# Performance work log

Measured on AMD Instinct MI355X. Metric: run time of the kernel, lower is better.

The kernel has to match this reference:

```python
import jax, jax.numpy as jnp
import numpy as np
from jax import lax

# hyperparams (match init_kwargs)
DIM = 192      # dim
QK = 192       # qk_dim
HEADS = 8
GS = 128       # group_size
MLP = 384      # mlp_dim
M = 64         # num_tokens
B, H, W = 4, 128, 128


def setup_inputs() -> dict:
    key = jax.random.key(0)
    ks = jax.random.split(key, 12)
    def n(k, sh, sc=0.02):
        return jax.random.normal(k, sh, dtype=jnp.float32) * sc
    return {
        "x": n(ks[0], (B, DIM, H, W), 1.0),
        "ln_g": jnp.ones((DIM,), jnp.float32),
        "ln_b": jnp.zeros((DIM,), jnp.float32),
        "Wq": n(ks[1], (DIM, QK)),
        "Wk": n(ks[2], (DIM, QK)),
        "Wv": n(ks[3], (DIM, DIM)),
        "Wproj": n(ks[4], (DIM, DIM)),
        "Wkg": n(ks[5], (DIM, QK)),      # IRCA global-key projection of means
        "Wvg": n(ks[6], (DIM, DIM)),     # IRCA global-value projection of means
        "means": n(ks[7], (M, DIM), 1.0),  # token dictionary buffer
        "Wconv": n(ks[8], (DIM, DIM)),   # 1x1 conv (no bias) as matrix
        "mlp_ln_g": jnp.ones((DIM,), jnp.float32),
        "mlp_ln_b": jnp.zeros((DIM,), jnp.float32),
        "W_fc1": n(ks[9], (DIM, MLP)),
        "dw": n(ks[10], (MLP, 1, 3, 3)),  # depthwise 3x3 in ConvFFN
        "W_fc2": n(ks[11], (MLP, DIM)),
    }


def _ln(x, g, b, eps=1e-5):
    mu = x.mean(-1, keepdims=True)
    var = ((x - mu) ** 2).mean(-1, keepdims=True)
    return (x - mu) * lax.rsqrt(var + eps) * g + b


def _attn(q, k, v):
    scale = q.shape[-1] ** -0.5
    s = jnp.einsum('...qd,...kd->...qk', q, k) * scale
    p = jax.nn.softmax(s, axis=-1)
    return jnp.einsum('...qk,...kd->...qd', p, v)


def reference(x, ln_g, ln_b, Wq, Wk, Wv, Wproj, Wkg, Wvg, means,
              Wconv, mlp_ln_g, mlp_ln_b, W_fc1, dw, W_fc2):
    b, C, h, w = x.shape
    N = h * w
    xt = x.reshape(b, C, N).transpose(0, 2, 1)          # b n c
    residual = xt
    xn = _ln(xt, ln_g, ln_b)

    # IRCA: per-head global K/V from the token dictionary (means)
    kg = (means @ Wkg).reshape(M, HEADS, QK // HEADS).transpose(1, 0, 2)   # h m dq
    vg = (means @ Wvg).reshape(M, HEADS, C // HEADS).transpose(1, 0, 2)    # h m dv

    # cluster assignment (no-grad): cosine sim to means, argsort by cluster id
    xs = lax.stop_gradient(xn)
    ms = lax.stop_gradient(means)
    xs_n = xs / (jnp.linalg.norm(xs, axis=-1, keepdims=True) + 1e-12)
    ms_n = ms / (jnp.linalg.norm(ms, axis=-1, keepdims=True) + 1e-12)
    belong = jnp.argmax(xs_n @ ms_n.T, axis=-1)          # b n
    idx = jnp.argsort(belong, axis=-1)                   # b n, cluster-sorted order

    # IASA: project, gather into cluster-sorted order
    q = jnp.take_along_axis(xn @ Wq, idx[:, :, None], axis=1)
    k = jnp.take_along_axis(xn @ Wk, idx[:, :, None], axis=1)
    v = jnp.take_along_axis(xn @ Wv, idx[:, :, None], axis=1)

    gs = min(N, GS)
    ng = (N + gs - 1) // gs
    pad_n = ng * gs - N
    pq = jnp.concatenate([q, q[:, N - pad_n:N][:, ::-1]], axis=1)
    pq = pq.reshape(b, ng, gs, HEADS, -1).transpose(0, 1, 3, 2, 4)  # b ng h gs dq

    def windows(t):
        tr = jnp.concatenate([t, t[:, N - pad_n - gs:N][:, ::-1]], axis=1)  # len ng*gs+gs
        t1 = tr[:, :ng * gs].reshape(b, ng, gs, -1)
        t2 = tr[:, gs:].reshape(b, ng, gs, -1)
        tw = jnp.concatenate([t1, t2], axis=2)           # b ng 2gs c
        return tw.reshape(b, ng, 2 * gs, HEADS, -1).transpose(0, 1, 3, 2, 4)

    kw, vw = windows(k), windows(v)
    out1 = _attn(pq, kw, vw)                             # local overlapping windows
    out2 = _attn(pq, kg[None, None], vg[None, None])     # global dictionary attention
    out = (out1 + out2).transpose(0, 1, 3, 2, 4).reshape(b, ng * gs, C)[:, :N]

    # scatter back to original token order (idx is a permutation)
    inv = jnp.argsort(idx, axis=-1)
    out = jnp.take_along_axis(out, inv[:, :, None], axis=1)
    out = (out @ Wproj) @ Wconv                           # proj + 1x1 conv (no bias)
    xt = residual + out

    # PreNorm ConvFFN: LN -> fc1 -> depthwise 3x3 -> GELU -> fc2, residual
    h1 = _ln(xt, mlp_ln_g, mlp_ln_b) @ W_fc1              # b n mlp
    himg = h1.transpose(0, 2, 1).reshape(b, MLP, h, w)
    dwc = lax.conv_general_dilated(himg, dw, (1, 1), 'SAME',
                                   feature_group_count=MLP,
                                   dimension_numbers=('NCHW', 'OIHW', 'NCHW'))
    h2 = jax.nn.gelu(dwc.reshape(b, MLP, N).transpose(0, 2, 1))
    xt = xt + h2 @ W_fc2
    return xt.transpose(0, 2, 1).reshape(b, C, h, w)
```

## Files before the change

### kernel.cpp

```cpp
#include <hip/hip_runtime.h>

using u16 = unsigned short;
using u32 = unsigned int;
typedef __attribute__((ext_vector_type(8))) short short8;
typedef __attribute__((ext_vector_type(4))) short s16x4;
typedef __attribute__((ext_vector_type(4))) float f32x4;
typedef __attribute__((ext_vector_type(2))) float f32x2;
typedef __attribute__((ext_vector_type(4))) u16 u16x4;
typedef __attribute__((ext_vector_type(4))) u32 u32x4;

constexpr int CB   = 4;
constexpr int CC   = 192;
constexpr int CN   = 16384;
constexpr int BN   = CB * CN;
constexpr int CMLP = 384;

__device__ __forceinline__ float b2f(u16 u){ return __uint_as_float(((u32)u) << 16); }
__device__ __forceinline__ u16 f2b(float f){
  u32 u = __float_as_uint(f);
  u32 r = (u + 0x7FFFu + ((u >> 16) & 1u)) >> 16;
  return (u16)r;
}
__device__ __forceinline__ short8 ld8(const u16* p) {
  s16x4 a = *(const s16x4*)p;
  s16x4 b = *(const s16x4*)(p + 4);
  short8 r;
  r[0]=a[0]; r[1]=a[1]; r[2]=a[2]; r[3]=a[3];
  r[4]=b[0]; r[5]=b[1]; r[6]=b[2]; r[7]=b[3];
  return r;
}
__device__ __forceinline__ u32 pk_bf16(float lo, float hi) {
  u32 r;
  asm("v_cvt_pk_bf16_f32 %0, %1, %2" : "=v"(r) : "v"(lo), "v"(hi));
  return r;
}
__device__ __forceinline__ float exp2_fast(float x) {
  float r;
  asm("v_exp_f32 %0, %1" : "=v"(r) : "v"(x));
  return r;
}

template<int SRCMAJ>
__global__ __launch_bounds__(256) void ln_k(const float* __restrict__ src,
    const float* __restrict__ gg, const float* __restrict__ bb, u16* __restrict__ out,
    const u16* __restrict__ msnT, int* __restrict__ belong)
{
  __shared__ float t[64 * 193];
  __shared__ float sg[192], sb[192];
  __shared__ float smu[64], srs[64];
  const int tid = threadIdx.x;
  const int blk = blockIdx.x;
  const int b = blk >> 8;
  const int n0 = (blk & 255) * 64;
  if (tid < 192) { sg[tid] = gg[tid]; sb[tid] = bb[tid]; }
  if (SRCMAJ == 0) {
    const size_t sbase = ((size_t)b * CC) * CN + n0;
    #pragma unroll
    for (int it = 0; it < 48; ++it) {
      int c = it * 4 + (tid >> 6);
      int tok = tid & 63;
      t[tok * 193 + c] = src[sbase + (size_t)c * CN + tok];
    }
  } else {
    const size_t sbase = ((size_t)(b * CN + n0)) * CC;
    #pragma unroll
    for (int it = 0; it < 48; ++it) {
      int e = it * 256 + tid;
      int tok = e / 192, c = e % 192;
      t[tok * 193 + c] = src[sbase + (size_t)tok * CC + c];
    }
  }
  __syncthreads();
  {
    int tok = tid >> 2, sub = tid & 3;
    float s = 0.f, sq = 0.f;
    #pragma unroll
    for (int i = 0; i < 48; ++i) {
      float v = t[tok * 193 + sub * 48 + i];
      s += v; sq += v * v;
    }
    s  += __shfl_xor(s, 1);  s  += __shfl_xor(s, 2);
    sq += __shfl_xor(sq, 1); sq += __shfl_xor(sq, 2);
    float mu = s * (1.f / 192.f);
    float var = fmaxf(sq * (1.f / 192.f) - mu * mu, 0.f);
    float rs = rsqrtf(var + 1e-5f);
    if (sub == 0) { smu[tok] = mu; srs[tok] = rs; }
  }
  __syncthreads();
  const size_t obase = ((size_t)(b * CN + n0)) * CC;
  #pragma unroll
  for (int it = 0; it < 48; ++it) {
    int e = it * 256 + tid;
    int tk = e / 192, c = e % 192;
    float v = (t[tk * 193 + c] - smu[tk]) * srs[tk] * sg[c] + sb[c];
    out[obase + (size_t)tk * CC + c] = f2b(v);
  }

  if (SRCMAJ == 0) {
    const int wv = tid >> 6, lane = tid & 63;
    const int l15 = lane & 15, g4 = lane >> 4, q8 = g4 * 8;
    const int tok = wv * 16 + l15;
    const float mu = smu[tok], rs = srs[tok];
    short8 afm[6];
    #pragma unroll
    for (int ks = 0; ks < 6; ++ks) {
      u32x4 qq;
      #pragma unroll
      for (int j = 0; j < 4; ++j) {
        int c = ks * 32 + q8 + 2 * j;
        float v0 = (t[tok * 193 + c]     - mu) * rs * sg[c]     + sb[c];
        float v1 = (t[tok * 193 + c + 1] - mu) * rs * sg[c + 1] + sb[c + 1];
        qq[j] = pk_bf16(v0, v1);
      }
      afm[ks] = __builtin_bit_cast(short8, qq);
    }
    f32x4 sacc[4];
    #pragma unroll
    for (int ct = 0; ct < 4; ++ct) {
      sacc[ct] = 0.f;
      const u16* pM = msnT + (ct * 16 + l15) * 192 + q8;
      short8 mf[6];
      #pragma unroll
      for (int ks = 0; ks < 6; ++ks) mf[ks] = *(const short8*)(pM + ks * 32);
      #pragma unroll
      for (int ks = 0; ks < 6; ++ks)
        sacc[ct] = __builtin_amdgcn_mfma_f32_16x16x32_bf16(afm[ks], mf[ks], sacc[ct], 0, 0, 0);
    }
    #pragma unroll
    for (int r = 0; r < 4; ++r) {
      float bv = -3e38f; int bi = 1 << 30;
      #pragma unroll
      for (int ct = 0; ct < 4; ++ct) {
        float v = sacc[ct][r];
        int ci = ct * 16 + l15;
        if (v > bv || (v == bv && ci < bi)) { bv = v; bi = ci; }
      }
      #pragma unroll
      for (int d = 1; d < 16; d <<= 1) {
        float ov = __shfl_xor(bv, d);
        int   oi = __shfl_xor(bi, d);
        if (ov > bv || (ov == bv && oi < bi)) { bv = ov; bi = oi; }
      }
      if (l15 == 0) belong[b * CN + n0 + wv * 16 + g4 * 4 + r] = bi;
    }
  }
}

__global__ __launch_bounds__(192) void prep_means_k(const float* __restrict__ means,
    const float* __restrict__ Wkg, const float* __restrict__ Wvg,
    u16* __restrict__ msnT, float* __restrict__ kg, float* __restrict__ vg)
{
  __shared__ float sv[192];
  __shared__ float red[192];
  const int m = blockIdx.x, c = threadIdx.x;
  float v = means[m * 192 + c];
  sv[c] = v; red[c] = v * v;
  __syncthreads();
  for (int s = 96; s >= 3; s >>= 1) {
    if (c < s) red[c] += red[c + s];
    __syncthreads();
  }
  if (c == 0) red[0] = 1.f / (sqrtf(red[0] + red[1] + red[2]) + 1e-12f);
  __syncthreads();
  float scale = red[0];
  msnT[m * 192 + c] = f2b(v * scale);
  float a1 = 0.f, a2 = 0.f;
  for (int cc = 0; cc < 192; ++cc) {
    float mv = sv[cc];
    a1 += mv * Wkg[cc * 192 + c];
    a2 += mv * Wvg[cc * 192 + c];
  }
  int h = c / 24, d = c % 24;
  kg[h * (64 * 24) + m * 24 + d] = a1;
  vg[h * (64 * 24) + m * 24 + d] = a2;
}

__global__ __launch_bounds__(256) void wpcT_k(const float* __restrict__ Wp,
    const float* __restrict__ Wc, u16* __restrict__ WpcT)
{
  int e = blockIdx.x * 256 + threadIdx.x;
  if (e >= 192 * 192) return;
  int i = e / 192, j = e % 192;
  float a = 0.f;
  for (int k = 0; k < 192; ++k) a += Wp[i * 192 + k] * Wc[k * 192 + j];
  WpcT[j * 192 + i] = f2b(a);
}

__global__ __launch_bounds__(256) void wT_k(const float* __restrict__ W,
    u16* __restrict__ dst, int K, int NCsrc, int jcount)
{
  int e = blockIdx.x * 256 + threadIdx.x;
  if (e >= K * jcount) return;
  int j = e / K, k = e % K;
  dst[e] = f2b(W[k * NCsrc + j]);
}

enum { EP_QKV = 0, EP_RESID = 2, EP_H1 = 3, EP_FINAL = 4 };

template<int KTOT, int NCOLS, int EPI>
__global__ __launch_bounds__(256) void gemm3_k(const u16* __restrict__ A,
    const u16* __restrict__ Wt, const float* __restrict__ resid,
    void* __restrict__ outp, int astride)
{
  __shared__ __attribute__((aligned(16))) u16 lA[64 * 200];
  constexpr int KC = KTOT / 192;
  constexpr int WCOLS = NCOLS / 4;
  constexpr int WCT = WCOLS / 16;
  constexpr int NACC = (KC == 2) ? WCT * 4 : 4;
  const int tid = threadIdx.x;
  const int row0 = blockIdx.y * 64;
  const int b = row0 >> 14;
  const int col0 = blockIdx.x * NCOLS;
  const int wv = tid >> 6, lane = tid & 63;
  const int l15 = lane & 15, g4 = lane >> 4, q8 = g4 * 8;
  const int colw = col0 + wv * WCOLS;

  f32x4 acc[NACC];
  #pragma unroll
  for (int i = 0; i < NACC; ++i) acc[i] = 0.f;

  #pragma unroll
  for (int kc = 0; kc < KC; ++kc) {
    if (kc) __syncthreads();
    #pragma unroll
    for (int it = 0; it < 12; ++it) {
      int e4 = (it * 256 + tid) * 4;
      int r = e4 / 192, k = e4 % 192;
      u16x4 v = *(const u16x4*)(A + (size_t)(row0 + r) * astride + kc * 192 + k);
      *(u16x4*)(lA + r * 200 + k) = v;
    }
    __syncthreads();
    short8 af[4][6];
    #pragma unroll
    for (int rt = 0; rt < 4; ++rt)
      #pragma unroll
      for (int ks = 0; ks < 6; ++ks)
        af[rt][ks] = *(const short8*)(lA + (rt * 16 + l15) * 200 + ks * 32 + q8);

    #pragma unroll
    for (int jc = 0; jc < WCT; ++jc) {
      const u16* pW = Wt + (size_t)(colw + jc * 16 + l15) * KTOT + kc * 192 + q8;
      short8 wf[6];
      #pragma unroll
      for (int ks = 0; ks < 6; ++ks) wf[ks] = *(const short8*)(pW + ks * 32);
      #pragma unroll
      for (int ks = 0; ks < 6; ++ks)
        #pragma unroll
        for (int rt = 0; rt < 4; ++rt) {
          int ai = (KC == 2) ? jc * 4 + rt : rt;
          if (EPI == EP_FINAL)
            acc[ai] = __builtin_amdgcn_mfma_f32_16x16x32_bf16(wf[ks], af[rt][ks], acc[ai], 0, 0, 0);
          else
            acc[ai] = __builtin_amdgcn_mfma_f32_16x16x32_bf16(af[rt][ks], wf[ks], acc[ai], 0, 0, 0);
        }

      if (KC == 1 && EPI == EP_QKV) {
        u16* o = (u16*)outp;
        int col = colw + jc * 16 + l15;
        #pragma unroll
        for (int rt = 0; rt < 4; ++rt) {
          int row = row0 + rt * 16 + g4 * 4;
          #pragma unroll
          for (int r = 0; r < 4; ++r)
            o[(size_t)(row + r) * 576 + col] = f2b(acc[rt][r]);
          acc[rt] = 0.f;
        }
      } else if (KC == 1 && EPI == EP_H1) {
        u16* o = (u16*)outp;
        int col = colw + jc * 16 + l15;
        #pragma unroll
        for (int rt = 0; rt < 4; ++rt) {
          int row = row0 + rt * 16 + g4 * 4;
          #pragma unroll
          for (int r = 0; r < 4; ++r)
            o[(size_t)(row + r) * CMLP + col] = f2b(acc[rt][r]);
          acc[rt] = 0.f;
        }
      } else if (KC == 1 && EPI == EP_RESID) {
        float* o = (float*)outp;
        int col = colw + jc * 16 + l15;
        size_t cb = ((size_t)(b * CC + col)) * CN;
        #pragma unroll
        for (int rt = 0; rt < 4; ++rt) {
          int row = row0 + rt * 16 + g4 * 4;
          #pragma unroll
          for (int r = 0; r < 4; ++r) {
            int n = (row + r) & 16383;
            o[(size_t)(row + r) * CC + col] = resid[cb + n] + acc[rt][r];
          }
          acc[rt] = 0.f;
        }
      }
    }
  }

  if (EPI == EP_FINAL) {
    float* o = (float*)outp;
    #pragma unroll
    for (int jc = 0; jc < WCT; ++jc)
      #pragma unroll
      for (int tt = 0; tt < 4; ++tt) {
        int token = row0 + tt * 16 + l15;
        int n = token & 16383;
        #pragma unroll
        for (int r = 0; r < 4; ++r) {
          int outcol = colw + jc * 16 + g4 * 4 + r;
          o[((size_t)(b * CC + outcol)) * CN + n] =
              resid[(size_t)token * CC + outcol] + acc[jc * 4 + tt][r];
        }
      }
  }
}

__global__ __launch_bounds__(256) void hist_k(const int* __restrict__ belong, int* __restrict__ histG)
{
  __shared__ int h[64];
  int tid = threadIdx.x, blk = blockIdx.x;
  if (tid < 64) h[tid] = 0;
  __syncthreads();
  int c = belong[blk * 256 + tid];
  atomicAdd(&h[c], 1);
  __syncthreads();
  if (tid < 64) histG[blk * 64 + tid] = h[tid];
}

__global__ __launch_bounds__(64) void scan_k(const int* __restrict__ histG, int* __restrict__ chunkBase)
{
  int b = blockIdx.x, c = threadIdx.x;
  int tot = 0;
  for (int ch = 0; ch < 64; ++ch) tot += histG[(b * 64 + ch) * 64 + c];
  int inc = tot;
  for (int d = 1; d < 64; d <<= 1) {
    int v = __shfl_up(inc, d);
    if (c >= d) inc += v;
  }
  int run = inc - tot;
  for (int ch = 0; ch < 64; ++ch) {
    chunkBase[(b * 64 + ch) * 64 + c] = run;
    run += histG[(b * 64 + ch) * 64 + c];
  }
}

__global__ __launch_bounds__(256) void rank_k(const int* __restrict__ belong,
    const int* __restrict__ chunkBase, int* __restrict__ idx)
{
  __shared__ int WH[4][64];
  int tid = threadIdx.x, blk = blockIdx.x;
  int b = blk >> 6, chl = blk & 63;
  int wv = tid >> 6, lane = tid & 63;
  ((int*)WH)[tid] = 0;
  __syncthreads();
  int nl = chl * 256 + tid;
  int c = belong[blk * 256 + tid];
  int rank = 0;
  for (int m = 0; m < 64; ++m) {
    unsigned long long msk = __ballot(c == m);
    if (c == m) {
      rank = __popcll(msk & ((1ull << lane) - 1ull));
      if (rank == 0) WH[wv][m] = __popcll(msk);
    }
  }
  __syncthreads();
  int off = 0;
  #pragma unroll
  for (int w = 0; w < 3; ++w) if (w < wv) off += WH[w][c];
  int pos = chunkBase[(b * 64 + chl) * 64 + c] + off + rank;
  idx[b * CN + pos] = nl;
}

__global__ __launch_bounds__(256) void attn_k(u16* __restrict__ qkv,
    const float* __restrict__ kg, const float* __restrict__ vg,
    const int* __restrict__ idx)
{
  __shared__ __attribute__((aligned(16))) u16 sK[320 * 28];
  __shared__ __attribute__((aligned(16))) u16 sVT[24 * 340];
  __shared__ int sidx[256];
  const int g = blockIdx.x, h = blockIdx.y, b = blockIdx.z;
  const int tid = threadIdx.x;
  const int wave = tid >> 6, lane = tid & 63;
  const int l15 = lane & 15, g4 = lane >> 4;
  const int q8 = g4 * 8;
  const size_t base = (size_t)b * CN * 576;
  const float QSC = 0.20412414523193154f * 1.4426950408889634f;
  short8 z8 = {0,0,0,0,0,0,0,0};

  {
    int p = g * 128 + tid;
    if (p >= CN) p = 2 * CN - 1 - p;
    sidx[tid] = idx[b * CN + p];
  }
  __syncthreads();

  #pragma unroll
  for (int it = 0; it < 8; ++it) {
    int e4 = (it * 256 + tid) * 4;
    if (e4 < 7680) {
      int r = e4 / 24, c = e4 % 24;
      if (r < 256) {
        int p = sidx[r];
        *(u16x4*)(sK + r * 28 + c) =
          *(const u16x4*)(qkv + base + (size_t)p * 576 + 192 + h * 24 + c);
      } else {
        const float* kp = kg + h * 1536 + (r - 256) * 24 + c;
        u16x4 o;
        o[0] = f2b(kp[0]); o[1] = f2b(kp[1]); o[2] = f2b(kp[2]); o[3] = f2b(kp[3]);
        *(u16x4*)(sK + r * 28 + c) = o;
      }
    }
  }
  #pragma unroll
  for (int it = 0; it < 8; ++it) {
    int e4 = (it * 256 + tid) * 4;
    if (e4 < 7680) {
      int kk = e4 / 24, c = e4 % 24;
      if (kk < 256) {
        int p = sidx[kk];
        u16x4 v = *(const u16x4*)(qkv + base + (size_t)p * 576 + 384 + h * 24 + c);
        sVT[(c + 0) * 340 + kk] = v[0];
        sVT[(c + 1) * 340 + kk] = v[1];
        sVT[(c + 2) * 340 + kk] = v[2];
        sVT[(c + 3) * 340 + kk] = v[3];
      } else {
        const float* vp = vg + h * 1536 + (kk - 256) * 24 + c;
        sVT[(c + 0) * 340 + kk] = f2b(vp[0]);
        sVT[(c + 1) * 340 + kk] = f2b(vp[1]);
        sVT[(c + 2) * 340 + kk] = f2b(vp[2]);
        sVT[(c + 3) * 340 + kk] = f2b(vp[3]);
      }
    }
  }

  short8 qf[2];
  #pragma unroll
  for (int rt = 0; rt < 2; ++rt) {
    int qrow = sidx[wave * 32 + rt * 16 + l15];
    if (g4 < 3) {
      short8 raw = ld8(qkv + base + (size_t)qrow * 576 + h * 24 + q8);
      u32x4 qq;
      #pragma unroll
      for (int j = 0; j < 4; ++j) {
        float lo = b2f((u16)raw[2 * j]) * QSC;
        float hi = b2f((u16)raw[2 * j + 1]) * QSC;
        qq[j] = pk_bf16(lo, hi);
      }
      qf[rt] = __builtin_bit_cast(short8, qq);
    } else {
      qf[rt] = z8;
    }
  }
  __syncthreads();

  float l1[2] = {0.f, 0.f}, l2[2] = {0.f, 0.f};
  f32x4 O1[2][2], O2[2][2];
  #pragma unroll
  for (int rt = 0; rt < 2; ++rt)
    #pragma unroll
    for (int ct2 = 0; ct2 < 2; ++ct2) { O1[rt][ct2] = 0.f; O2[rt][ct2] = 0.f; }

  const int srow = (lane & 48) + ((lane & 48) >> 2);
  const int srcLo = ((lane & 16) << 1) + l15;
  const int srcHi = srcLo + 16;
  const bool hiSel = lane >= 32;
  f32x4 zz = 0.f;

  auto do_tile = [&](int ktile, float* l, f32x4 (*O)[2]) {
    short8 aK[4];
    #pragma unroll
    for (int ct = 0; ct < 4; ++ct)
      aK[ct] = (g4 < 3) ? ld8(sK + (ktile + ct * 16 + l15) * 28 + q8) : z8;
    short8 bV[2][2];
    #pragma unroll
    for (int kc = 0; kc < 2; ++kc)
      #pragma unroll
      for (int ct2 = 0; ct2 < 2; ++ct2) {
        int vrow = ct2 * 16 + l15;
        bV[kc][ct2] = (vrow < 24) ? ld8(sVT + vrow * 340 + ktile + kc * 32 + q8) : z8;
      }
    #pragma unroll
    for (int rt = 0; rt < 2; ++rt) {
      f32x4 p[4];
      #pragma unroll
      for (int ct = 0; ct < 4; ++ct)
        p[ct] = __builtin_amdgcn_mfma_f32_16x16x32_bf16(aK[ct], qf[rt], zz, 0, 0, 0);
      float ps = 0.f;
      #pragma unroll
      for (int ct = 0; ct < 4; ++ct)
        #pragma unroll
        for (int r = 0; r < 4; ++r) {
          float pe = exp2_fast(p[ct][r]);
          p[ct][r] = pe;
          ps += pe;
        }
      ps += __shfl_xor(ps, 16);
      ps += __shfl_xor(ps, 32);
      l[rt] += ps;
      #pragma unroll
      for (int kc = 0; kc < 2; ++kc) {
        u32 wA0 = pk_bf16(p[kc * 2][0], p[kc * 2][1]);
        u32 wA1 = pk_bf16(p[kc * 2][2], p[kc * 2][3]);
        u32 wB0 = pk_bf16(p[kc * 2 + 1][0], p[kc * 2 + 1][1]);
        u32 wB1 = pk_bf16(p[kc * 2 + 1][2], p[kc * 2 + 1][3]);
        u32 a0 = (u32)__shfl((int)wA0, srcLo), a1 = (u32)__shfl((int)wA1, srcLo);
        u32 a2 = (u32)__shfl((int)wA0, srcHi), a3 = (u32)__shfl((int)wA1, srcHi);
        u32 b0 = (u32)__shfl((int)wB0, srcLo), b1 = (u32)__shfl((int)wB1, srcLo);
        u32 b2 = (u32)__shfl((int)wB0, srcHi), b3 = (u32)__shfl((int)wB1, srcHi);
        u32x4 fr;
        fr[0] = hiSel ? b0 : a0; fr[1] = hiSel ? b1 : a1;
        fr[2] = hiSel ? b2 : a2; fr[3] = hiSel ? b3 : a3;
        short8 aP = __builtin_bit_cast(short8, fr);
        #pragma unroll
        for (int ct2 = 0; ct2 < 2; ++ct2)
          O[rt][ct2] = __builtin_amdgcn_mfma_f32_16x16x32_bf16(aP, bV[kc][ct2], O[rt][ct2], 0, 0, 0);
      }
    }
  };

  do_tile(0,   l1, O1);
  do_tile(64,  l1, O1);
  do_tile(128, l1, O1);
  do_tile(192, l1, O1);
  do_tile(256, l2, O2);

  #pragma unroll
  for (int rt = 0; rt < 2; ++rt) {
    float li1 = 1.f / l1[rt];
    float li2 = 1.f / l2[rt];
    #pragma unroll
    for (int r = 0; r < 4; ++r) {
      float i1 = __shfl(li1, srow + r);
      float i2 = __shfl(li2, srow + r);
      int tok = sidx[wave * 32 + rt * 16 + g4 * 4 + r];
      #pragma unroll
      for (int ct2 = 0; ct2 < 2; ++ct2) {
        int d = ct2 * 16 + l15;
        if (d < 24) {
          float v = O1[rt][ct2][r] * i1 + O2[rt][ct2][r] * i2;
          qkv[base + (size_t)tok * 576 + h * 24 + d] = f2b(v);
        }
      }
    }
  }
}

__global__ __launch_bounds__(256) void conv_k(const u16* __restrict__ h1,
    const float* __restrict__ dw, u16* __restrict__ h2g)
{
  __shared__ float t[1156 * 10];
  __shared__ float sdw[72];
  const int tile = blockIdx.x;
  const int jg = blockIdx.y;
  const int bb = blockIdx.z;
  const int y0 = (tile >> 2) * 32, x0 = (tile & 3) * 32;
  const int tid = threadIdx.x;
  if (tid < 72) sdw[tid] = dw[jg * 72 + tid];
  #pragma unroll
  for (int it = 0; it < 5; ++it) {
    int e = it * 256 + tid;
    if (e < 1156) {
      int yy = e / 34 - 1 + y0, xx = e % 34 - 1 + x0;
      float v[8];
      if (yy >= 0 && yy < 128 && xx >= 0 && xx < 128) {
        short8 raw = *(const short8*)(h1 + ((size_t)(bb * CN + yy * 128 + xx)) * CMLP + jg * 8);
        #pragma unroll
        for (int c = 0; c < 8; ++c) v[c] = b2f((u16)raw[c]);
      } else {
        #pragma unroll
        for (int c = 0; c < 8; ++c) v[c] = 0.f;
      }
      #pragma unroll
      for (int c = 0; c < 8; c += 2) {
        f32x2 p; p[0] = v[c]; p[1] = v[c + 1];
        *(f32x2*)(t + e * 10 + c) = p;
      }
    }
  }
  __syncthreads();
  float acc[4][8];
  #pragma unroll
  for (int px = 0; px < 4; ++px)
    #pragma unroll
    for (int c = 0; c < 8; ++c) acc[px][c] = 0.f;
  #pragma unroll
  for (int k = 0; k < 9; ++k) {
    const int dy = k / 3, dx = k % 3;
    float w[8];
    #pragma unroll
    for (int c = 0; c < 8; ++c) w[c] = sdw[c * 9 + k];
    #pragma unroll
    for (int px = 0; px < 4; ++px) {
      int idx2 = px * 256 + tid;
      int oy = idx2 >> 5, ox = idx2 & 31;
      const float* vp = t + ((oy + dy) * 34 + ox + dx) * 10;
      #pragma unroll
      for (int c = 0; c < 8; ++c) acc[px][c] += vp[c] * w[c];
    }
  }
  #pragma unroll
  for (int px = 0; px < 4; ++px) {
    int idx2 = px * 256 + tid;
    int oy = idx2 >> 5, ox = idx2 & 31;
    short8 o;
    #pragma unroll
    for (int c = 0; c < 8; ++c) {
      float a = acc[px][c];
      float u = 1.5957691216057308f * (a + 0.044715f * a * a * a);
      float gel = a / (1.f + __expf(-u));
      o[c] = (short)f2b(gel);
    }
    *(short8*)(h2g + ((size_t)(bb * CN + (y0 + oy) * 128 + x0 + ox)) * CMLP + jg * 8) = o;
  }
}

extern "C" void kernel_launch(void* const* d_in, const int* in_sizes, int n_in,
                              void* d_out, int out_size, void* d_ws, size_t ws_size,
                              hipStream_t stream)
{
  const float* x     = (const float*)d_in[0];
  const float* ln_g  = (const float*)d_in[1];
  const float* ln_b  = (const float*)d_in[2];
  const float* Wq    = (const float*)d_in[3];
  const float* Wk    = (const float*)d_in[4];
  const float* Wv    = (const float*)d_in[5];
  const float* Wproj = (const float*)d_in[6];
  const float* Wkg   = (const float*)d_in[7];
  const float* Wvg   = (const float*)d_in[8];
  const float* means = (const float*)d_in[9];
  const float* Wconv = (const float*)d_in[10];
  const float* mlp_g = (const float*)d_in[11];
  const float* mlp_b = (const float*)d_in[12];
  const float* Wfc1  = (const float*)d_in[13];
  const float* dw    = (const float*)d_in[14];
  const float* Wfc2  = (const float*)d_in[15];
  float* out = (float*)d_out;
  (void)in_sizes; (void)n_in; (void)out_size; (void)ws_size;

  char* ws = (char*)d_ws;
  size_t off = 0;
  auto alloc = [&](size_t sz) { void* p = ws + off; off += (sz + 255) & ~(size_t)255; return p; };
  u16*  xn    = (u16*)alloc((size_t)BN * 192 * 2);
  u16*  qkv   = (u16*)alloc((size_t)BN * 576 * 2);
  float* xt2  = (float*)alloc((size_t)BN * 192 * 4);
  u16*  h2g   = (u16*)alloc((size_t)BN * 384 * 2);
  u16*  msnT  = (u16*)alloc(64 * 192 * 2);
  u16*  WqkvT = (u16*)alloc(576 * 192 * 2);
  u16*  WpcT  = (u16*)alloc(192 * 192 * 2);
  u16*  Wfc1T = (u16*)alloc(384 * 192 * 2);
  u16*  Wfc2T = (u16*)alloc(192 * 384 * 2);
  float* kg   = (float*)alloc(8 * 64 * 24 * 4);
  float* vg   = (float*)alloc(8 * 64 * 24 * 4);
  int*  belong = (int*)alloc(BN * 4);
  int*  idxb   = (int*)alloc(BN * 4);
  int*  histG  = (int*)alloc(256 * 64 * 4);
  int*  chunkBase = (int*)alloc(256 * 64 * 4);
  u16* ln2 = xn;
  u16* h1  = qkv;

  prep_means_k<<<64, 192, 0, stream>>>(means, Wkg, Wvg, msnT, kg, vg);
  wpcT_k<<<144, 256, 0, stream>>>(Wproj, Wconv, WpcT);
  wT_k<<<144, 256, 0, stream>>>(Wq, WqkvT + 0,             192, 192, 192);
  wT_k<<<144, 256, 0, stream>>>(Wk, WqkvT + 192 * 192,     192, 192, 192);
  wT_k<<<144, 256, 0, stream>>>(Wv, WqkvT + 2 * 192 * 192, 192, 192, 192);
  wT_k<<<288, 256, 0, stream>>>(Wfc1, Wfc1T, 192, 384, 384);
  wT_k<<<288, 256, 0, stream>>>(Wfc2, Wfc2T, 384, 192, 192);

  ln_k<0><<<1024, 256, 0, stream>>>(x, ln_g, ln_b, xn, msnT, belong);
  hist_k<<<256, 256, 0, stream>>>(belong, histG);
  scan_k<<<4, 64, 0, stream>>>(histG, chunkBase);
  rank_k<<<256, 256, 0, stream>>>(belong, chunkBase, idxb);
  gemm3_k<192, 192, EP_QKV><<<dim3(3, 1024), 256, 0, stream>>>(xn, WqkvT, nullptr, qkv, 192);
  attn_k<<<dim3(128, 8, 4), 256, 0, stream>>>(qkv, kg, vg, idxb);
  gemm3_k<192, 192, EP_RESID><<<dim3(1, 1024), 256, 0, stream>>>(qkv, WpcT, x, xt2, 576);
  ln_k<1><<<1024, 256, 0, stream>>>(xt2, mlp_g, mlp_b, ln2, nullptr, nullptr);
  gemm3_k<192, 192, EP_H1><<<dim3(2, 1024), 256, 0, stream>>>(ln2, Wfc1T, nullptr, h1, 192);
  conv_k<<<dim3(16, 48, 4), 256, 0, stream>>>(h1, dw, h2g);
  gemm3_k<384, 192, EP_FINAL><<<dim3(1, 1024), 256, 0, stream>>>(h2g, Wfc2T, xt2, out, 384);
}
```

Before: 372.4 us.

## Use async global-to-LDS loads, channel-major xt2, and wider GEMM column tiles

The GEMM A-tile staging now uses global_load_lds 16-byte direct copies into an unpadded LDS tile instead of register round-trips into a padded one. The residual GEMM now writes xt2 channel-major, with swapped MFMA operands, so the second LayerNorm and the final GEMM read it with coalesced accesses. The QKV and fc1 GEMMs each become a single block per row tile covering all output columns, so the A tile is loaded once rather than three or two times. Removing the LDS padding may add bank conflicts on the fragment reads, and the wider column tiles add per-wave work and register pressure.

```diff
diff --git a/kernel.cpp b/kernel.cpp
--- a/kernel.cpp
+++ b/kernel.cpp
@@ -39,8 +39,13 @@
   asm("v_exp_f32 %0, %1" : "=v"(r) : "v"(x));
   return r;
 }
-
-template<int SRCMAJ>
+__device__ __forceinline__ void gl_lds16(const u16* g, u16* l) {
+  __builtin_amdgcn_global_load_lds(
+      (const __attribute__((address_space(1))) void*)(const void*)g,
+      (__attribute__((address_space(3))) void*)(void*)l, 16, 0, 0);
+}
+
+template<int DOARG>
 __global__ __launch_bounds__(256) void ln_k(const float* __restrict__ src,
     const float* __restrict__ gg, const float* __restrict__ bb, u16* __restrict__ out,
     const u16* __restrict__ msnT, int* __restrict__ belong)
@@ -53,22 +58,12 @@
   const int b = blk >> 8;
   const int n0 = (blk & 255) * 64;
   if (tid < 192) { sg[tid] = gg[tid]; sb[tid] = bb[tid]; }
-  if (SRCMAJ == 0) {
-    const size_t sbase = ((size_t)b * CC) * CN + n0;
-    #pragma unroll
-    for (int it = 0; it < 48; ++it) {
-      int c = it * 4 + (tid >> 6);
-      int tok = tid & 63;
-      t[tok * 193 + c] = src[sbase + (size_t)c * CN + tok];
-    }
-  } else {
-    const size_t sbase = ((size_t)(b * CN + n0)) * CC;
-    #pragma unroll
-    for (int it = 0; it < 48; ++it) {
-      int e = it * 256 + tid;
-      int tok = e / 192, c = e % 192;
-      t[tok * 193 + c] = src[sbase + (size_t)tok * CC + c];
-    }
+  const size_t sbase = ((size_t)b * CC) * CN + n0;
+  #pragma unroll
+  for (int it = 0; it < 48; ++it) {
+    int c = it * 4 + (tid >> 6);
+    int tok = tid & 63;
+    t[tok * 193 + c] = src[sbase + (size_t)c * CN + tok];
   }
   __syncthreads();
   {
@@ -96,7 +91,7 @@
     out[obase + (size_t)tk * CC + c] = f2b(v);
   }
 
-  if (SRCMAJ == 0) {
+  if (DOARG) {
     const int wv = tid >> 6, lane = tid & 63;
     const int l15 = lane & 15, g4 = lane >> 4, q8 = g4 * 8;
     const int tok = wv * 16 + l15;
@@ -202,7 +197,7 @@
     const u16* __restrict__ Wt, const float* __restrict__ resid,
     void* __restrict__ outp, int astride)
 {
-  __shared__ __attribute__((aligned(16))) u16 lA[64 * 200];
+  __shared__ __attribute__((aligned(16))) u16 lA[64 * 192];
   constexpr int KC = KTOT / 192;
   constexpr int WCOLS = NCOLS / 4;
   constexpr int WCT = WCOLS / 16;
@@ -223,11 +218,12 @@
   for (int kc = 0; kc < KC; ++kc) {
     if (kc) __syncthreads();
     #pragma unroll
-    for (int it = 0; it < 12; ++it) {
-      int e4 = (it * 256 + tid) * 4;
-      int r = e4 / 192, k = e4 % 192;
-      u16x4 v = *(const u16x4*)(A + (size_t)(row0 + r) * astride + kc * 192 + k);
-      *(u16x4*)(lA + r * 200 + k) = v;
+    for (int j = 0; j < 6; ++j) {
+      int C = (wv * 6 + j) * 64 + lane;
+      int r = C / 24;
+      int c = C - r * 24;
+      const u16* gp = A + (size_t)(row0 + r) * astride + kc * 192 + c * 8;
+      gl_lds16(gp, lA + (wv * 6 + j) * 512);
     }
     __syncthreads();
     short8 af[4][6];
@@ -235,7 +231,7 @@
     for (int rt = 0; rt < 4; ++rt)
       #pragma unroll
       for (int ks = 0; ks < 6; ++ks)
-        af[rt][ks] = *(const short8*)(lA + (rt * 16 + l15) * 200 + ks * 32 + q8);
+        af[rt][ks] = *(const short8*)(lA + (rt * 16 + l15) * 192 + ks * 32 + q8);
 
     #pragma unroll
     for (int jc = 0; jc < WCT; ++jc) {
@@ -248,7 +244,7 @@
         #pragma unroll
         for (int rt = 0; rt < 4; ++rt) {
           int ai = (KC == 2) ? jc * 4 + rt : rt;
-          if (EPI == EP_FINAL)
+          if (EPI == EP_FINAL || EPI == EP_RESID)
             acc[ai] = __builtin_amdgcn_mfma_f32_16x16x32_bf16(wf[ks], af[rt][ks], acc[ai], 0, 0, 0);
           else
             acc[ai] = __builtin_amdgcn_mfma_f32_16x16x32_bf16(af[rt][ks], wf[ks], acc[ai], 0, 0, 0);
@@ -278,15 +274,14 @@
         }
       } else if (KC == 1 && EPI == EP_RESID) {
         float* o = (float*)outp;
-        int col = colw + jc * 16 + l15;
-        size_t cb = ((size_t)(b * CC + col)) * CN;
         #pragma unroll
         for (int rt = 0; rt < 4; ++rt) {
-          int row = row0 + rt * 16 + g4 * 4;
+          int n = ((row0 + rt * 16) & 16383) + l15;
           #pragma unroll
           for (int r = 0; r < 4; ++r) {
-            int n = (row + r) & 16383;
-            o[(size_t)(row + r) * CC + col] = resid[cb + n] + acc[rt][r];
+            int col = colw + jc * 16 + g4 * 4 + r;
+            size_t o2 = ((size_t)(b * CC + col)) * CN + n;
+            o[o2] = resid[o2] + acc[rt][r];
           }
           acc[rt] = 0.f;
         }
@@ -300,13 +295,12 @@
     for (int jc = 0; jc < WCT; ++jc)
       #pragma unroll
       for (int tt = 0; tt < 4; ++tt) {
-        int token = row0 + tt * 16 + l15;
-        int n = token & 16383;
+        int n = ((row0 + tt * 16) & 16383) + l15;
         #pragma unroll
         for (int r = 0; r < 4; ++r) {
           int outcol = colw + jc * 16 + g4 * 4 + r;
-          o[((size_t)(b * CC + outcol)) * CN + n] =
-              resid[(size_t)token * CC + outcol] + acc[jc * 4 + tt][r];
+          size_t o2 = ((size_t)(b * CC + outcol)) * CN + n;
+          o[o2] = resid[o2] + acc[jc * 4 + tt][r];
         }
       }
   }
@@ -663,15 +657,15 @@
   wT_k<<<288, 256, 0, stream>>>(Wfc1, Wfc1T, 192, 384, 384);
   wT_k<<<288, 256, 0, stream>>>(Wfc2, Wfc2T, 384, 192, 192);
 
-  ln_k<0><<<1024, 256, 0, stream>>>(x, ln_g, ln_b, xn, msnT, belong);
+  ln_k<1><<<1024, 256, 0, stream>>>(x, ln_g, ln_b, xn, msnT, belong);
   hist_k<<<256, 256, 0, stream>>>(belong, histG);
   scan_k<<<4, 64, 0, stream>>>(histG, chunkBase);
   rank_k<<<256, 256, 0, stream>>>(belong, chunkBase, idxb);
-  gemm3_k<192, 192, EP_QKV><<<dim3(3, 1024), 256, 0, stream>>>(xn, WqkvT, nullptr, qkv, 192);
+  gemm3_k<192, 576, EP_QKV><<<dim3(1, 1024), 256, 0, stream>>>(xn, WqkvT, nullptr, qkv, 192);
   attn_k<<<dim3(128, 8, 4), 256, 0, stream>>>(qkv, kg, vg, idxb);
   gemm3_k<192, 192, EP_RESID><<<dim3(1, 1024), 256, 0, stream>>>(qkv, WpcT, x, xt2, 576);
-  ln_k<1><<<1024, 256, 0, stream>>>(xt2, mlp_g, mlp_b, ln2, nullptr, nullptr);
-  gemm3_k<192, 192, EP_H1><<<dim3(2, 1024), 256, 0, stream>>>(ln2, Wfc1T, nullptr, h1, 192);
+  ln_k<0><<<1024, 256, 0, stream>>>(xt2, mlp_g, mlp_b, ln2, nullptr, nullptr);
+  gemm3_k<192, 384, EP_H1><<<dim3(1, 1024), 256, 0, stream>>>(ln2, Wfc1T, nullptr, h1, 192);
   conv_k<<<dim3(16, 48, 4), 256, 0, stream>>>(h1, dw, h2g);
   gemm3_k<384, 192, EP_FINAL><<<dim3(1, 1024), 256, 0, stream>>>(h2g, Wfc2T, xt2, out, 384);
 }
```

After: 344.4 us. 7.5% less time.
